# Optimization experiments

Hardware: AMD Instinct MI355X
Metric: run time of the kernel (lower is better)

## Reference

```python
import jax, jax.numpy as jnp
import numpy as np

N = 1048576
DIM = 2
HID = 64
E = 4


def setup_inputs() -> dict:
    key = jax.random.key(0)
    ks = jax.random.split(key, 10)
    s_in = 1.0 / np.sqrt(DIM)
    s_hid = 1.0 / np.sqrt(HID)
    return {
        "x": jax.random.normal(ks[0], (N, DIM), dtype=jnp.float32),
        # router: Linear(dim -> E)
        "rW": jax.random.uniform(ks[1], (DIM, E), minval=-s_in, maxval=s_in, dtype=jnp.float32),
        "rb": jax.random.uniform(ks[2], (E,), minval=-s_in, maxval=s_in, dtype=jnp.float32),
        # stacked expert weights: Linear(dim->hid), Linear(hid->hid), Linear(hid->dim)
        "w1": jax.random.uniform(ks[3], (E, DIM, HID), minval=-s_in, maxval=s_in, dtype=jnp.float32),
        "b1": jax.random.uniform(ks[4], (E, HID), minval=-s_in, maxval=s_in, dtype=jnp.float32),
        "w2": jax.random.uniform(ks[5], (E, HID, HID), minval=-s_hid, maxval=s_hid, dtype=jnp.float32),
        "b2": jax.random.uniform(ks[6], (E, HID), minval=-s_hid, maxval=s_hid, dtype=jnp.float32),
        "w3": jax.random.uniform(ks[7], (E, HID, DIM), minval=-s_hid, maxval=s_hid, dtype=jnp.float32),
        "b3": jax.random.uniform(ks[8], (E, DIM), minval=-s_hid, maxval=s_hid, dtype=jnp.float32),
    }


def reference(x, rW, rb, w1, b1, w2, b2, w3, b3):
    # Router: hard top-1 via argmax, exactly as torch.argmax(router_logits, -1)
    router_logits = x @ rW + rb                       # [N, E]
    best = jnp.argmax(router_logits, axis=-1)         # [N]

    # Compute all experts densely (vectorized replacement of the masked loop),
    # then select the winning expert's output per token via one-hot.
    h = jax.nn.relu(jnp.einsum('nd,edh->enh', x, w1) + b1[:, None, :])   # [E, N, HID]
    h = jax.nn.relu(jnp.einsum('enh,ehk->enk', h, w2) + b2[:, None, :])  # [E, N, HID]
    y = jnp.einsum('enh,ehd->end', h, w3) + b3[:, None, :]               # [E, N, DIM]

    onehot = jax.nn.one_hot(best, E, dtype=x.dtype)   # [N, E]
    out = jnp.einsum('end,ne->nd', y, onehot)         # [N, DIM]
    return out, router_logits
```

## Files before the change

kernel.cpp:

```cpp
#include <hip/hip_runtime.h>

#define NTOK 1048576
#define HID 64
#define TPB 256
#define TPB_TOK 1024
#define RPT (TPB_TOK / TPB)
#define NBLK (NTOK / TPB_TOK)
#define MAXSLOT (TPB_TOK + 64)
#define MAXTILE (TPB_TOK / 16 + 4)

typedef _Float16 half8 __attribute__((ext_vector_type(8)));
typedef _Float16 half2v __attribute__((ext_vector_type(2)));
typedef float f32x4 __attribute__((ext_vector_type(4)));

static __device__ __forceinline__ half2v pkh(float a, float b) {
    return __builtin_bit_cast(half2v, __builtin_amdgcn_cvt_pkrtz(a, b));
}

__global__ void prep_w2_frag(const float* __restrict__ w2, _Float16* __restrict__ wsf) {
    int idx  = blockIdx.x * 256 + threadIdx.x;
    int j    = idx & 7;
    int lane = (idx >> 3) & 63;
    int ks   = (idx >> 9) & 1;
    int mt   = (idx >> 10) & 3;
    int e    = idx >> 12;
    int kin  = ks * 32 + (lane >> 4) * 8 + j;
    int m    = mt * 16 + (lane & 15);
    wsf[idx] = (_Float16)w2[(e * HID + kin) * HID + m];
}

__global__ __launch_bounds__(TPB, 4) void moe_kernel(
    const float* __restrict__ x, const float* __restrict__ rW, const float* __restrict__ rb,
    const float* __restrict__ w1, const float* __restrict__ b1,
    const float* __restrict__ b2,
    const float* __restrict__ w3, const float* __restrict__ b3,
    const _Float16* __restrict__ wsf, float* __restrict__ out)
{
    __shared__ float2 xs[MAXSLOT];
    __shared__ float2 ysh[MAXSLOT];
    __shared__ int wcnt[4][4];
    __shared__ int seg_start[4], cumt[5];
    __shared__ unsigned tmap[MAXTILE];

    const int t = threadIdx.x, w = t >> 6, lane = t & 63;
    const int base = blockIdx.x * TPB_TOK;
    const unsigned long long lt = (1ull << lane) - 1ull;

    const float r00 = rW[0], r01 = rW[1], r02 = rW[2], r03 = rW[3];
    const float r10 = rW[4], r11 = rW[5], r12 = rW[6], r13 = rW[7];
    const float rb0 = rb[0], rb1 = rb[1], rb2 = rb[2], rb3 = rb[3];

    int c0 = 0, c1 = 0, c2 = 0, c3 = 0;
    int slotl[RPT]; int bestl[RPT]; float2 xv_[RPT]; int slotf[RPT];
    float* logits_out = out + 2 * NTOK;
    #pragma unroll
    for (int i = 0; i < RPT; i++) {
        int tok = base + i * TPB + t;
        float2 xv = ((const float2*)x)[tok];
        float l0 = xv.x * r00 + xv.y * r10 + rb0;
        float l1 = xv.x * r01 + xv.y * r11 + rb1;
        float l2 = xv.x * r02 + xv.y * r12 + rb2;
        float l3 = xv.x * r03 + xv.y * r13 + rb3;
        ((float4*)logits_out)[tok] = make_float4(l0, l1, l2, l3);
        int b = 0; float bv = l0;
        if (l1 > bv) { bv = l1; b = 1; }
        if (l2 > bv) { bv = l2; b = 2; }
        if (l3 > bv) { bv = l3; b = 3; }
        unsigned long long m0 = __ballot(b == 0), m1 = __ballot(b == 1),
                           m2 = __ballot(b == 2), m3 = __ballot(b == 3);
        unsigned long long mym = (b == 0) ? m0 : (b == 1) ? m1 : (b == 2) ? m2 : m3;
        int cb = (b == 0) ? c0 : (b == 1) ? c1 : (b == 2) ? c2 : c3;
        slotl[i] = cb + __popcll(mym & lt);
        bestl[i] = b; xv_[i] = xv;
        c0 += __popcll(m0); c1 += __popcll(m1); c2 += __popcll(m2); c3 += __popcll(m3);
    }
    if (lane < 4) wcnt[w][lane] = (lane == 0) ? c0 : (lane == 1) ? c1 : (lane == 2) ? c2 : c3;
    __syncthreads();
    if (t == 0) {
        int run = 0, ct = 0; cumt[0] = 0;
        for (int e = 0; e < 4; e++) {
            int c = wcnt[0][e] + wcnt[1][e] + wcnt[2][e] + wcnt[3][e];
            seg_start[e] = run;
            run += (c + 15) & ~15; ct += (c + 15) >> 4; cumt[e + 1] = ct;
        }
    }
    __syncthreads();
    int wo0 = 0, wo1 = 0, wo2 = 0, wo3 = 0;
    for (int ww = 0; ww < w; ww++) {
        wo0 += wcnt[ww][0]; wo1 += wcnt[ww][1]; wo2 += wcnt[ww][2]; wo3 += wcnt[ww][3];
    }
    #pragma unroll
    for (int i = 0; i < RPT; i++) {
        int b = bestl[i];
        int wo = (b == 0) ? wo0 : (b == 1) ? wo1 : (b == 2) ? wo2 : wo3;
        int slot = seg_start[b] + wo + slotl[i];
        xs[slot] = xv_[i];
        slotf[i] = slot;
    }
    int T = cumt[4];
    for (int g = t; g < T; g += TPB) {
        int e = (g >= cumt[1]) + (g >= cumt[2]) + (g >= cumt[3]);
        int i = g - cumt[e];
        int row = seg_start[e] + 16 * i;
        tmap[g] = (unsigned)e | ((unsigned)row << 2);
    }
    __syncthreads();

    const int q = lane >> 4, n16 = lane & 15;
    int chunk = (T + 3) >> 2;
    int g0 = w * chunk, g1 = g0 + chunk; if (g1 > T) g1 = T;

    half2v w1h0[8], w1h1[8], b1h[8];
    half8 w2A[4][2];
    half2v b2h[4][2];
    half2v w3h[4][4];
    float2 b3r = make_float2(0.f, 0.f);
    int cur_e = -1;
    const half2v hz = { (_Float16)0, (_Float16)0 };

    unsigned tm_n = 0; float2 xv_n = make_float2(0.f, 0.f);
    if (g0 < g1) {
        tm_n = tmap[g0];
        xv_n = xs[((tm_n >> 2) & 0xFFF) + n16];
    }

    for (int g = g0; g < g1; g++) {
        unsigned tm = tm_n; float2 xv = xv_n;
        if (g + 1 < g1) {
            tm_n = tmap[g + 1];
            xv_n = xs[((tm_n >> 2) & 0xFFF) + n16];
        }
        int e   = tm & 3;
        int row = (tm >> 2) & 0xFFF;
        if (e != cur_e) {
            cur_e = e;
            const float* base0 = w1 + e * 128;
            const float* base1 = w1 + e * 128 + 64;
            const float* baseb = b1 + e * 64;
            #pragma unroll
            for (int p = 0; p < 4; p++) {
                float2 a0 = *(const float2*)(base0 + q * 8 + 2 * p);
                float2 a1 = *(const float2*)(base0 + 32 + q * 8 + 2 * p);
                w1h0[p]     = pkh(a0.x, a0.y);
                w1h0[4 + p] = pkh(a1.x, a1.y);
                float2 c0_ = *(const float2*)(base1 + q * 8 + 2 * p);
                float2 c1_ = *(const float2*)(base1 + 32 + q * 8 + 2 * p);
                w1h1[p]     = pkh(c0_.x, c0_.y);
                w1h1[4 + p] = pkh(c1_.x, c1_.y);
                float2 d0 = *(const float2*)(baseb + q * 8 + 2 * p);
                float2 d1 = *(const float2*)(baseb + 32 + q * 8 + 2 * p);
                b1h[p]     = pkh(d0.x, d0.y);
                b1h[4 + p] = pkh(d1.x, d1.y);
            }
            #pragma unroll
            for (int mt = 0; mt < 4; mt++) {
                w2A[mt][0] = ((const half8*)wsf)[((e * 4 + mt) * 2 + 0) * 64 + lane];
                w2A[mt][1] = ((const half8*)wsf)[((e * 4 + mt) * 2 + 1) * 64 + lane];
                float4 bb = ((const float4*)(b2 + e * 64))[mt * 4 + q];
                b2h[mt][0] = pkh(bb.x, bb.y);
                b2h[mt][1] = pkh(bb.z, bb.w);
                #pragma unroll
                for (int i = 0; i < 4; i++) {
                    int r = mt * 16 + q * 4 + i;
                    float2 wv = ((const float2*)(w3 + e * 128))[r];
                    w3h[mt][i] = pkh(wv.x, wv.y);
                }
            }
            b3r = ((const float2*)b3)[e];
        }
        half2v xh0 = pkh(xv.x, xv.x);
        half2v xh1 = pkh(xv.y, xv.y);
        half8 bf0, bf1;
        #pragma unroll
        for (int p = 0; p < 4; p++) {
            half2v ha = w1h0[p] * xh0 + w1h1[p] * xh1 + b1h[p];
            half2v hb = w1h0[4 + p] * xh0 + w1h1[4 + p] * xh1 + b1h[4 + p];
            ha = __builtin_elementwise_max(ha, hz);
            hb = __builtin_elementwise_max(hb, hz);
            bf0[2 * p] = ha.x; bf0[2 * p + 1] = ha.y;
            bf1[2 * p] = hb.x; bf1[2 * p + 1] = hb.y;
        }
        half2v ya = hz, yb = hz;
        #pragma unroll
        for (int mt = 0; mt < 4; mt++) {
            f32x4 acc = {0.f, 0.f, 0.f, 0.f};
            acc = __builtin_amdgcn_mfma_f32_16x16x32_f16(w2A[mt][0], bf0, acc, 0, 0, 0);
            acc = __builtin_amdgcn_mfma_f32_16x16x32_f16(w2A[mt][1], bf1, acc, 0, 0, 0);
            half2v h01 = __builtin_elementwise_max(pkh(acc[0], acc[1]) + b2h[mt][0], hz);
            half2v h23 = __builtin_elementwise_max(pkh(acc[2], acc[3]) + b2h[mt][1], hz);
            half2v h0s = { h01.x, h01.x }, h1s = { h01.y, h01.y };
            half2v h2s = { h23.x, h23.x }, h3s = { h23.y, h23.y };
            half2v* acc01 = (mt & 2) ? &yb : &ya;
            *acc01 = *acc01 + h0s * w3h[mt][0];
            *acc01 = *acc01 + h1s * w3h[mt][1];
            *acc01 = *acc01 + h2s * w3h[mt][2];
            *acc01 = *acc01 + h3s * w3h[mt][3];
        }
        half2v yp = ya + yb;
        float yr = __builtin_bit_cast(float, yp);
        yp = yp + __builtin_bit_cast(half2v, __shfl_xor(yr, 16));
        yr = __builtin_bit_cast(float, yp);
        yp = yp + __builtin_bit_cast(half2v, __shfl_xor(yr, 32));
        if (q == 0) {
            ysh[row + n16] = make_float2((float)yp.x + b3r.x, (float)yp.y + b3r.y);
        }
    }
    __syncthreads();

    #pragma unroll
    for (int i = 0; i < RPT; i++) {
        ((float2*)out)[base + i * TPB + t] = ysh[slotf[i]];
    }
}

extern "C" void kernel_launch(void* const* d_in, const int* in_sizes, int n_in,
                              void* d_out, int out_size, void* d_ws, size_t ws_size,
                              hipStream_t stream) {
    const float* x  = (const float*)d_in[0];
    const float* rW = (const float*)d_in[1];
    const float* rb = (const float*)d_in[2];
    const float* w1 = (const float*)d_in[3];
    const float* b1 = (const float*)d_in[4];
    const float* w2 = (const float*)d_in[5];
    const float* b2 = (const float*)d_in[6];
    const float* w3 = (const float*)d_in[7];
    const float* b3 = (const float*)d_in[8];
    float* out = (float*)d_out;
    _Float16* wsf = (_Float16*)d_ws;

    hipLaunchKernelGGL(prep_w2_frag, dim3(64), dim3(256), 0, stream, w2, wsf);
    hipLaunchKernelGGL(moe_kernel, dim3(NBLK), dim3(TPB), 0, stream,
                       x, rW, rb, w1, b1, b2, w3, b3, (const _Float16*)wsf, out);
}
```

Measured before the change: 103.1 us.

## Drop w2 fragment prep kernel and use nontemporal output stores

Removes the separate prep kernel that repacked w2 into fp16 MFMA fragments. Each wave now gathers and converts its w2 fragment straight from the fp32 global weights when it switches expert. Logits and output stores are also made nontemporal so they do not pollute the cache. This saves one kernel launch and the dependency between the two kernels, at the cost of strided scalar global loads for w2 inside the main kernel.

```diff
diff --git a/kernel.cpp b/kernel.cpp
--- a/kernel.cpp
+++ b/kernel.cpp
@@ -12,32 +12,21 @@
 typedef _Float16 half8 __attribute__((ext_vector_type(8)));
 typedef _Float16 half2v __attribute__((ext_vector_type(2)));
 typedef float f32x4 __attribute__((ext_vector_type(4)));
+typedef float f32x2 __attribute__((ext_vector_type(2)));
 
 static __device__ __forceinline__ half2v pkh(float a, float b) {
     return __builtin_bit_cast(half2v, __builtin_amdgcn_cvt_pkrtz(a, b));
 }
 
-__global__ void prep_w2_frag(const float* __restrict__ w2, _Float16* __restrict__ wsf) {
-    int idx  = blockIdx.x * 256 + threadIdx.x;
-    int j    = idx & 7;
-    int lane = (idx >> 3) & 63;
-    int ks   = (idx >> 9) & 1;
-    int mt   = (idx >> 10) & 3;
-    int e    = idx >> 12;
-    int kin  = ks * 32 + (lane >> 4) * 8 + j;
-    int m    = mt * 16 + (lane & 15);
-    wsf[idx] = (_Float16)w2[(e * HID + kin) * HID + m];
-}
-
 __global__ __launch_bounds__(TPB, 4) void moe_kernel(
     const float* __restrict__ x, const float* __restrict__ rW, const float* __restrict__ rb,
     const float* __restrict__ w1, const float* __restrict__ b1,
-    const float* __restrict__ b2,
+    const float* __restrict__ w2, const float* __restrict__ b2,
     const float* __restrict__ w3, const float* __restrict__ b3,
-    const _Float16* __restrict__ wsf, float* __restrict__ out)
+    float* __restrict__ out)
 {
     __shared__ float2 xs[MAXSLOT];
-    __shared__ float2 ysh[MAXSLOT];
+    __shared__ f32x2 ysh[MAXSLOT];
     __shared__ int wcnt[4][4];
     __shared__ int seg_start[4], cumt[5];
     __shared__ unsigned tmap[MAXTILE];
@@ -61,7 +50,8 @@
         float l1 = xv.x * r01 + xv.y * r11 + rb1;
         float l2 = xv.x * r02 + xv.y * r12 + rb2;
         float l3 = xv.x * r03 + xv.y * r13 + rb3;
-        ((float4*)logits_out)[tok] = make_float4(l0, l1, l2, l3);
+        f32x4 lv = { l0, l1, l2, l3 };
+        __builtin_nontemporal_store(lv, (f32x4*)logits_out + tok);
         int b = 0; float bv = l0;
         if (l1 > bv) { bv = l1; b = 1; }
         if (l2 > bv) { bv = l2; b = 2; }
@@ -152,10 +142,16 @@
                 b1h[p]     = pkh(d0.x, d0.y);
                 b1h[4 + p] = pkh(d1.x, d1.y);
             }
+            const float* w2e = w2 + e * 64 * 64 + (q * 8) * 64 + (n16);
             #pragma unroll
             for (int mt = 0; mt < 4; mt++) {
-                w2A[mt][0] = ((const half8*)wsf)[((e * 4 + mt) * 2 + 0) * 64 + lane];
-                w2A[mt][1] = ((const half8*)wsf)[((e * 4 + mt) * 2 + 1) * 64 + lane];
+                half8 f0, f1;
+                #pragma unroll
+                for (int j = 0; j < 8; j++) {
+                    f0[j] = (_Float16)w2e[j * 64 + mt * 16];
+                    f1[j] = (_Float16)w2e[32 * 64 + j * 64 + mt * 16];
+                }
+                w2A[mt][0] = f0; w2A[mt][1] = f1;
                 float4 bb = ((const float4*)(b2 + e * 64))[mt * 4 + q];
                 b2h[mt][0] = pkh(bb.x, bb.y);
                 b2h[mt][1] = pkh(bb.z, bb.w);
@@ -202,14 +198,15 @@
         yr = __builtin_bit_cast(float, yp);
         yp = yp + __builtin_bit_cast(half2v, __shfl_xor(yr, 32));
         if (q == 0) {
-            ysh[row + n16] = make_float2((float)yp.x + b3r.x, (float)yp.y + b3r.y);
+            f32x2 yo = { (float)yp.x + b3r.x, (float)yp.y + b3r.y };
+            ysh[row + n16] = yo;
         }
     }
     __syncthreads();
 
     #pragma unroll
     for (int i = 0; i < RPT; i++) {
-        ((float2*)out)[base + i * TPB + t] = ysh[slotf[i]];
+        __builtin_nontemporal_store(ysh[slotf[i]], (f32x2*)out + base + i * TPB + t);
     }
 }
 
@@ -226,9 +223,7 @@
     const float* w3 = (const float*)d_in[7];
     const float* b3 = (const float*)d_in[8];
     float* out = (float*)d_out;
-    _Float16* wsf = (_Float16*)d_ws;
-
-    hipLaunchKernelGGL(prep_w2_frag, dim3(64), dim3(256), 0, stream, w2, wsf);
+
     hipLaunchKernelGGL(moe_kernel, dim3(NBLK), dim3(TPB), 0, stream,
-                       x, rW, rb, w1, b1, b2, w3, b3, (const _Float16*)wsf, out);
+                       x, rW, rb, w1, b1, w2, b2, w3, b3, out);
 }
```

Measured after the change: 106.9 us. +3.7%, slower.
